# Performance work log

Measured on AMD Instinct MI355X. Metric: run time of the kernel, lower is better.

## Reference

```python
import jax, jax.numpy as jnp
import numpy as np

CH = 128
GROUPS = 8
EPS = 1e-5


def setup_inputs() -> dict:
    key = jax.random.key(0)
    ks = jax.random.split(key, 12)
    b, c, h, w = 16, CH, 64, 64
    x = jax.random.normal(ks[0], (b, c, h, w), dtype=jnp.float32)
    s = 1.0 / np.sqrt(c)
    return {
        "x": x,
        "gn_w": jnp.ones((c,), jnp.float32),
        "gn_b": jnp.zeros((c,), jnp.float32),
        "wq": jax.random.normal(ks[1], (c, c), jnp.float32) * s,
        "bq": jax.random.normal(ks[2], (c,), jnp.float32) * 0.01,
        "wk": jax.random.normal(ks[3], (c, c), jnp.float32) * s,
        "bk": jax.random.normal(ks[4], (c,), jnp.float32) * 0.01,
        "wv": jax.random.normal(ks[5], (c, c), jnp.float32) * s,
        "bv": jax.random.normal(ks[6], (c,), jnp.float32) * 0.01,
        "wf": jax.random.normal(ks[7], (c, c), jnp.float32) * s,
        "bf": jax.random.normal(ks[8], (c,), jnp.float32) * 0.01,
    }


def _group_norm(x, gamma, beta):
    b, c, h, w = x.shape
    xg = x.reshape(b, GROUPS, -1)  # [b, g, (c/g)*h*w]
    mean = xg.mean(axis=-1, keepdims=True)
    var = xg.var(axis=-1, keepdims=True)
    xn = ((xg - mean) * jax.lax.rsqrt(var + EPS)).reshape(b, c, h, w)
    return xn * gamma[None, :, None, None] + beta[None, :, None, None]


def reference(x, gn_w, gn_b, wq, bq, wk, bk, wv, bv, wf, bf):
    b, c, h, w = x.shape
    x_gn = _group_norm(x, gn_w, gn_b)
    xf = x_gn.reshape(b, c, h * w)  # [b, c, n]
    # 1x1 convs == per-position channel matmuls
    q = jnp.einsum('oc,bcn->bon', wq, xf) + bq[None, :, None]
    k = jnp.einsum('oc,bcn->bon', wk, xf) + bk[None, :, None]
    v = jnp.einsum('oc,bcn->bon', wv, xf) + bv[None, :, None]
    scale = c ** (-0.5)
    attn = jnp.einsum('bci,bcj->bij', q, k) * scale  # [b, n, n]
    attn = jax.nn.softmax(attn, axis=-1)
    # out[b,c,i] = sum_j v[b,c,j] * attn[b,i,j]
    o = jnp.einsum('bcj,bij->bci', v, attn)
    of = jnp.einsum('oc,bcn->bon', wf, o) + bf[None, :, None]
    return of.reshape(b, c, h, w) + x
```

## Files before the change

### kernel.cpp

```cpp
#include <hip/hip_runtime.h>

#define NB   16
#define NC   128
#define NPOS 4096

typedef short bf16x8 __attribute__((ext_vector_type(8)));
typedef float f32x4  __attribute__((ext_vector_type(4)));
typedef float f32x16 __attribute__((ext_vector_type(16)));
typedef unsigned int u32x4 __attribute__((ext_vector_type(4)));

#define SCF 0.12751743075095855f

static __device__ __forceinline__ unsigned short f2bf(float f) {
    unsigned int u = __builtin_bit_cast(unsigned int, f);
    u += 0x7FFFu + ((u >> 16) & 1u);
    return (unsigned short)(u >> 16);
}

static __device__ __forceinline__ unsigned int pkbf(float hi, float lo) {
    return __builtin_amdgcn_perm(__builtin_bit_cast(unsigned int, hi),
                                 __builtin_bit_cast(unsigned int, lo), 0x07060302u);
}

static __device__ __forceinline__ float vmax16(const f32x16 v) {
    float a = fmaxf(fmaxf(v[0], v[1]), fmaxf(v[2], v[3]));
    float b = fmaxf(fmaxf(v[4], v[5]), fmaxf(v[6], v[7]));
    float c = fmaxf(fmaxf(v[8], v[9]), fmaxf(v[10], v[11]));
    float d = fmaxf(fmaxf(v[12], v[13]), fmaxf(v[14], v[15]));
    return fmaxf(fmaxf(a, b), fmaxf(c, d));
}

static __device__ __forceinline__ float vsum16(const float* p) {
    float a = (p[0] + p[1]) + (p[2] + p[3]);
    float b = (p[4] + p[5]) + (p[6] + p[7]);
    float c = (p[8] + p[9]) + (p[10] + p[11]);
    float d = (p[12] + p[13]) + (p[14] + p[15]);
    return (a + b) + (c + d);
}

static __device__ __forceinline__ void mk_bfrag_pair(const float* pp, bf16x8* dst, int h) {
    #pragma unroll
    for (int c2 = 0; c2 < 2; ++c2) {
        int rb = c2 * 8;
        unsigned int A0 = pkbf(pp[rb + 1], pp[rb + 0]);
        unsigned int A1 = pkbf(pp[rb + 3], pp[rb + 2]);
        unsigned int B0 = pkbf(pp[rb + 5], pp[rb + 4]);
        unsigned int B1 = pkbf(pp[rb + 7], pp[rb + 6]);
        unsigned int s0 = h ? A0 : B0, s1 = h ? A1 : B1;
        unsigned int r0 = __shfl_xor(s0, 32), r1 = __shfl_xor(s1, 32);
        u32x4 f;
        f[0] = h ? r0 : A0; f[1] = h ? r1 : A1;
        f[2] = h ? B0 : r0; f[3] = h ? B1 : r1;
        dst[c2] = __builtin_bit_cast(bf16x8, f);
    }
}

__global__ void wconv_kernel(const float* __restrict__ wq, const float* __restrict__ wk,
                             const float* __restrict__ wv, const float* __restrict__ wf,
                             unsigned short* __restrict__ oq, unsigned short* __restrict__ ok,
                             unsigned short* __restrict__ ov, unsigned short* __restrict__ of) {
    int i = blockIdx.x * 256 + threadIdx.x;
    oq[i] = f2bf(wq[i]); ok[i] = f2bf(wk[i]); ov[i] = f2bf(wv[i]); of[i] = f2bf(wf[i]);
}

__global__ void gnstat_kernel(const float* __restrict__ x, float* __restrict__ mean,
                              float* __restrict__ rstd) {
    int bg = blockIdx.x;
    const float* p = x + (size_t)bg * 65536;
    int t = threadIdx.x;
    float s = 0.f, q = 0.f;
    for (int it = 0; it < 64; ++it) {
        f32x4 v = *(const f32x4*)(p + it * 1024 + t * 4);
        s += v[0] + v[1] + v[2] + v[3];
        q += v[0] * v[0] + v[1] * v[1] + v[2] * v[2] + v[3] * v[3];
    }
    for (int m = 1; m < 64; m <<= 1) { s += __shfl_xor(s, m); q += __shfl_xor(q, m); }
    __shared__ float ls[4], lq[4];
    int w = t >> 6;
    if ((t & 63) == 0) { ls[w] = s; lq[w] = q; }
    __syncthreads();
    if (t == 0) {
        s = ls[0] + ls[1] + ls[2] + ls[3];
        q = lq[0] + lq[1] + lq[2] + lq[3];
        float mu  = s * (1.0f / 65536.0f);
        float var = q * (1.0f / 65536.0f) - mu * mu;
        mean[bg] = mu;
        rstd[bg] = rsqrtf(var + 1e-5f);
    }
}

__global__ __launch_bounds__(256) void qkv_kernel(
    const float* __restrict__ x, const float* __restrict__ gnw, const float* __restrict__ gnb,
    const float* __restrict__ mean, const float* __restrict__ rstd,
    const unsigned short* __restrict__ wqb, const unsigned short* __restrict__ wkb,
    const unsigned short* __restrict__ wvb,
    const float* __restrict__ bq, const float* __restrict__ bk, const float* __restrict__ bv,
    unsigned short* __restrict__ qT, unsigned short* __restrict__ Kf, unsigned short* __restrict__ Vf) {
    __shared__ __attribute__((aligned(16))) unsigned short xn[64 * 136];
    __shared__ __attribute__((aligned(16))) unsigned short bnc[64 * 128];
    const int b = blockIdx.y, i0 = blockIdx.x * 64, jt = blockIdx.x;
    const int t = threadIdx.x;
    {
        int iL = (t & 15) * 4;
        int cb = (t >> 4) * 2;
        for (int cg = 0; cg < 4; ++cg) {
            int c = cg * 32 + cb;
            int g = c >> 4;
            float mu = mean[b * 8 + g], rs = rstd[b * 8 + g];
            float ga0 = gnw[c] * rs,     be0 = gnb[c]     - mu * ga0;
            float ga1 = gnw[c + 1] * rs, be1 = gnb[c + 1] - mu * ga1;
            const float* p0 = x + ((size_t)(b * NC + c)) * NPOS + i0 + iL;
            f32x4 v0 = *(const f32x4*)p0;
            f32x4 v1 = *(const f32x4*)(p0 + NPOS);
            for (int e = 0; e < 4; ++e) {
                unsigned int u = (unsigned)f2bf(v0[e] * ga0 + be0) |
                                 ((unsigned)f2bf(v1[e] * ga1 + be1) << 16);
                *(unsigned int*)&xn[(iL + e) * 136 + c] = u;
            }
        }
    }
    __syncthreads();

    const int lane = t & 63, w = t >> 6, quad = lane >> 4, li = lane & 15;

    bf16x8 ax[4];
    for (int kc = 0; kc < 4; ++kc)
        ax[kc] = *(const bf16x8*)&xn[(w * 16 + li) * 136 + kc * 32 + quad * 8];

    for (int wt = 0; wt < 2; ++wt) {
        const unsigned short* W = wt ? wkb : wqb;
        const float* bias = wt ? bk : bq;
        const float osc = wt ? 1.0f : SCF;
        for (int nt = 0; nt < 8; ++nt) {
            f32x4 d = {0.f, 0.f, 0.f, 0.f};
            for (int kc = 0; kc < 4; ++kc) {
                bf16x8 bw = *(const bf16x8*)&W[(nt * 16 + li) * 128 + kc * 32 + quad * 8];
                d = __builtin_amdgcn_mfma_f32_16x16x32_bf16(ax[kc], bw, d, 0, 0, 0);
            }
            float bb = bias[nt * 16 + li];
            int o = nt * 16 + li;
            for (int rr = 0; rr < 4; ++rr) {
                int i = w * 16 + quad * 4 + rr;
                bnc[i * 128 + (((o >> 3) ^ (i & 7)) << 3) + (o & 7)] = f2bf((d[rr] + bb) * osc);
            }
        }
        __syncthreads();
        if (wt == 0) {
            unsigned short* dst = qT + ((size_t)b * NPOS + i0) * NC + t * 32;
            int i = t >> 2;
            for (int s = 0; s < 4; ++s) {
                int cc = (t & 3) * 4 + s;
                *(bf16x8*)(dst + s * 8) = *(const bf16x8*)&bnc[i * 128 + ((cc ^ (i & 7)) << 3)];
            }
        } else {
            unsigned short* dst = Kf + ((size_t)(b * 64 + jt)) * 8192 + t * 32;
            int F = t >> 4, jtile = F >> 3, kc = F & 7;
            for (int s = 0; s < 4; ++s) {
                int L = (t * 4 + s) & 63;
                int i = jtile * 32 + (L & 31);
                int cc = kc * 2 + (L >> 5);
                *(bf16x8*)(dst + s * 8) = *(const bf16x8*)&bnc[i * 128 + ((cc ^ (i & 7)) << 3)];
            }
        }
        __syncthreads();
    }

    bf16x8 av[2][4];
    for (int mt = 0; mt < 2; ++mt)
        for (int kc = 0; kc < 4; ++kc)
            av[mt][kc] = *(const bf16x8*)&wvb[((w * 2 + mt) * 16 + li) * 128 + kc * 32 + quad * 8];
    for (int nt = 0; nt < 4; ++nt) {
        bf16x8 bx[4];
        for (int kc = 0; kc < 4; ++kc)
            bx[kc] = *(const bf16x8*)&xn[(nt * 16 + li) * 136 + kc * 32 + quad * 8];
        for (int mt = 0; mt < 2; ++mt) {
            f32x4 d = {0.f, 0.f, 0.f, 0.f};
            for (int kc = 0; kc < 4; ++kc)
                d = __builtin_amdgcn_mfma_f32_16x16x32_bf16(av[mt][kc], bx[kc], d, 0, 0, 0);
            int o0 = (w * 2 + mt) * 16 + quad * 4;
            int j = nt * 16 + li;
            for (int rr = 0; rr < 4; ++rr) {
                int c = o0 + rr;
                bnc[c * 64 + (((j >> 3) ^ (c & 7)) << 3) + (j & 7)] = f2bf(d[rr] + bv[c]);
            }
        }
    }
    __syncthreads();
    {
        unsigned short* dst = Vf + ((size_t)(b * 64 + jt)) * 8192 + t * 32;
        int F = t >> 4, ct = F >> 2, kc2 = F & 3;
        for (int s = 0; s < 4; ++s) {
            int L = (t * 4 + s) & 63;
            int c = ct * 32 + (L & 31);
            int jc = kc2 * 2 + (L >> 5);
            *(bf16x8*)(dst + s * 8) = *(const bf16x8*)&bnc[c * 64 + ((jc ^ (c & 7)) << 3)];
        }
    }
}

__global__ __launch_bounds__(256, 2) void flash_kernel(
    const unsigned short* __restrict__ qT, const unsigned short* __restrict__ Kf,
    const unsigned short* __restrict__ Vf, const unsigned short* __restrict__ wfb,
    const float* __restrict__ bf_, const float* __restrict__ x, float* __restrict__ out) {
    const int idx = blockIdx.x;
    const int b = (idx & 7) * 2 + ((idx >> 3) & 1);
    const int rg = idx >> 4;
    const int t = threadIdx.x, lane = t & 63, w = t >> 6;
    const int il = lane & 31, h = lane >> 5;
    const int iw = (rg * 4 + w) * 32;

    bf16x8 qb[8];
    #pragma unroll
    for (int kc = 0; kc < 8; ++kc)
        qb[kc] = *(const bf16x8*)&qT[((size_t)b * NPOS + iw + il) * NC + kc * 16 + h * 8];

    float mr = -1e30f, lr = 0.f;
    f32x16 acc[4];
    #pragma unroll
    for (int ct = 0; ct < 4; ++ct)
        #pragma unroll
        for (int q = 0; q < 16; ++q) acc[ct][q] = 0.f;

    const unsigned short* kp = Kf + ((size_t)b * 64) * 8192 + lane * 8;
    const unsigned short* vp = Vf + ((size_t)b * 64) * 8192 + lane * 8;

    bf16x8 kf[16];
    #pragma unroll
    for (int m = 0; m < 16; ++m) kf[m] = *(const bf16x8*)(kp + m * 512);
    kp += 8192;

    for (int jt = 0; jt < 64; ++jt) {
        f32x16 st[2];
        #pragma unroll
        for (int u = 0; u < 2; ++u)
            #pragma unroll
            for (int q = 0; q < 16; ++q) st[u][q] = 0.f;
        #pragma unroll
        for (int kc = 0; kc < 8; ++kc) {
            st[0] = __builtin_amdgcn_mfma_f32_32x32x16_bf16(kf[kc],     qb[kc], st[0], 0, 0, 0);
            st[1] = __builtin_amdgcn_mfma_f32_32x32x16_bf16(kf[8 + kc], qb[kc], st[1], 0, 0, 0);
        }
        #pragma unroll
        for (int m = 0; m < 16; ++m) kf[m] = *(const bf16x8*)(kp + m * 512);
        kp += 8192;

        float mx = fmaxf(vmax16(st[0]), vmax16(st[1]));
        mx = fmaxf(mx, __shfl_xor(mx, 32));
        if (__any(mx > mr)) {
            float mn = fmaxf(mr, mx);
            float alpha = __builtin_amdgcn_exp2f(mr - mn);
            mr = mn;
            lr *= alpha;
            #pragma unroll
            for (int ct = 0; ct < 4; ++ct)
                #pragma unroll
                for (int q = 0; q < 16; ++q) acc[ct][q] *= alpha;
        }
        float mc = mr - 0.0028150156f;
        #pragma unroll
        for (int q = 0; q < 16; ++q) {
            st[0][q] = __builtin_amdgcn_exp2f(st[0][q] - mc);
            st[1][q] = __builtin_amdgcn_exp2f(st[1][q] - mc);
        }
        float rs = vsum16((const float*)&st[0]) + vsum16((const float*)&st[1]);
        rs += __shfl_xor(rs, 32);
        lr += rs;

        bf16x8 pfrag[4];
        mk_bfrag_pair((const float*)&st[0], &pfrag[0], h);
        mk_bfrag_pair((const float*)&st[1], &pfrag[2], h);

        bf16x8 vf[16];
        #pragma unroll
        for (int m = 0; m < 16; ++m) vf[m] = *(const bf16x8*)(vp + m * 512);
        vp += 8192;

        #pragma unroll
        for (int ct = 0; ct < 4; ++ct)
            #pragma unroll
            for (int kc2 = 0; kc2 < 4; ++kc2)
                acc[ct] = __builtin_amdgcn_mfma_f32_32x32x16_bf16(vf[ct * 4 + kc2], pfrag[kc2],
                                                                  acc[ct], 0, 0, 0);
    }

    bf16x8 obf[8];
    {
        float inv = __builtin_amdgcn_rcpf(lr) * 1.001953125f;
        #pragma unroll
        for (int ct = 0; ct < 4; ++ct) {
            float pp[16];
            #pragma unroll
            for (int q = 0; q < 16; ++q) pp[q] = acc[ct][q] * inv;
            mk_bfrag_pair(pp, &obf[ct * 2], h);
        }
    }

    #pragma unroll
    for (int ot = 0; ot < 4; ++ot) {
        bf16x8 wfA[8];
        #pragma unroll
        for (int kc = 0; kc < 8; ++kc)
            wfA[kc] = *(const bf16x8*)&wfb[(ot * 32 + il) * 128 + kc * 16 + h * 8];
        f32x16 d;
        #pragma unroll
        for (int q = 0; q < 16; ++q) d[q] = 0.f;
        #pragma unroll
        for (int kc = 0; kc < 8; ++kc)
            d = __builtin_amdgcn_mfma_f32_32x32x16_bf16(wfA[kc], obf[kc], d, 0, 0, 0);
        const int gi = iw + il;
        #pragma unroll
        for (int q = 0; q < 16; ++q) {
            int o = ot * 32 + (q & 3) + 8 * (q >> 2) + 4 * h;
            size_t a = ((size_t)(b * NC + o)) * NPOS + gi;
            out[a] = d[q] + bf_[o] + x[a];
        }
    }
}

extern "C" void kernel_launch(void* const* d_in, const int* in_sizes, int n_in,
                              void* d_out, int out_size, void* d_ws, size_t ws_size,
                              hipStream_t stream) {
    const float* x   = (const float*)d_in[0];
    const float* gnw = (const float*)d_in[1];
    const float* gnb = (const float*)d_in[2];
    const float* wq  = (const float*)d_in[3];
    const float* bq  = (const float*)d_in[4];
    const float* wk  = (const float*)d_in[5];
    const float* bk  = (const float*)d_in[6];
    const float* wv  = (const float*)d_in[7];
    const float* bv  = (const float*)d_in[8];
    const float* wf  = (const float*)d_in[9];
    const float* bf_ = (const float*)d_in[10];
    float* out = (float*)d_out;

    char* ws = (char*)d_ws;
    float* mean = (float*)(ws + 0);
    float* rstd = (float*)(ws + 512);
    unsigned short* wqb = (unsigned short*)(ws + 1024);
    unsigned short* wkb = wqb + 16384;
    unsigned short* wvb = wkb + 16384;
    unsigned short* wfb = wvb + 16384;
    unsigned short* qT  = (unsigned short*)(ws + 132096);
    unsigned short* Kf  = qT + (size_t)NB * NPOS * NC;
    unsigned short* Vf  = Kf + (size_t)NB * NPOS * NC;

    wconv_kernel<<<64, 256, 0, stream>>>(wq, wk, wv, wf, wqb, wkb, wvb, wfb);
    gnstat_kernel<<<128, 256, 0, stream>>>(x, mean, rstd);
    dim3 g(64, 16);
    qkv_kernel<<<g, 256, 0, stream>>>(x, gnw, gnb, mean, rstd, wqb, wkb, wvb, bq, bk, bv, qT, Kf, Vf);
    flash_kernel<<<512, 256, 0, stream>>>(qT, Kf, Vf, wfb, bf_, x, out);
}
```

Measured before the change: 341.5 us.

## Stage K/V tiles in double-buffered LDS via direct global-to-LDS loads

Each of the four waves used to load every K and V tile from global memory into its own registers. Now the block shares the tiles through a double-buffered LDS area filled with global_load_lds, and the next tile is prefetched while the current one is used. The MFMA sections are also wrapped in s_setprio. This cuts redundant global and L2 traffic and register pressure. In exchange it adds 64KB of LDS per block (which may limit occupancy at two blocks per CU), a __syncthreads per iteration, and LDS read latency inside the MFMA chains.

Measured after the change: 315.3 us. 7.7% less time.

```diff
diff --git a/kernel.cpp b/kernel.cpp
--- a/kernel.cpp
+++ b/kernel.cpp
@@ -52,6 +52,17 @@
         f[0] = h ? r0 : A0; f[1] = h ? r1 : A1;
         f[2] = h ? B0 : r0; f[3] = h ? B1 : r1;
         dst[c2] = __builtin_bit_cast(bf16x8, f);
+    }
+}
+
+static __device__ __forceinline__ void stage_tile(unsigned short* lds, const unsigned short* g,
+                                                  int t, int w) {
+    #pragma unroll
+    for (int c = 0; c < 4; ++c) {
+        __builtin_amdgcn_global_load_lds(
+            (const __attribute__((address_space(1))) unsigned int*)(g + c * 2048 + t * 8),
+            (__attribute__((address_space(3))) unsigned int*)(lds + c * 2048 + w * 512),
+            16, 0, 0);
     }
 }
 
@@ -202,6 +213,7 @@
     const unsigned short* __restrict__ qT, const unsigned short* __restrict__ Kf,
     const unsigned short* __restrict__ Vf, const unsigned short* __restrict__ wfb,
     const float* __restrict__ bf_, const float* __restrict__ x, float* __restrict__ out) {
+    __shared__ __attribute__((aligned(16))) unsigned short KV[2][2][8192];
     const int idx = blockIdx.x;
     const int b = (idx & 7) * 2 + ((idx >> 3) & 1);
     const int rg = idx >> 4;
@@ -209,6 +221,12 @@
     const int il = lane & 31, h = lane >> 5;
     const int iw = (rg * 4 + w) * 32;
 
+    const unsigned short* Kb = Kf + ((size_t)b * 64) * 8192;
+    const unsigned short* Vb = Vf + ((size_t)b * 64) * 8192;
+
+    stage_tile(&KV[0][0][0], Kb, t, w);
+    stage_tile(&KV[0][1][0], Vb, t, w);
+
     bf16x8 qb[8];
     #pragma unroll
     for (int kc = 0; kc < 8; ++kc)
@@ -221,28 +239,31 @@
         #pragma unroll
         for (int q = 0; q < 16; ++q) acc[ct][q] = 0.f;
 
-    const unsigned short* kp = Kf + ((size_t)b * 64) * 8192 + lane * 8;
-    const unsigned short* vp = Vf + ((size_t)b * 64) * 8192 + lane * 8;
-
-    bf16x8 kf[16];
-    #pragma unroll
-    for (int m = 0; m < 16; ++m) kf[m] = *(const bf16x8*)(kp + m * 512);
-    kp += 8192;
+    __syncthreads();
 
     for (int jt = 0; jt < 64; ++jt) {
+        const int cur = jt & 1;
+        const unsigned short* kl = &KV[cur][0][0] + lane * 8;
+        const unsigned short* vl = &KV[cur][1][0] + lane * 8;
+        if (jt < 63) {
+            stage_tile(&KV[cur ^ 1][0][0], Kb + (size_t)(jt + 1) * 8192, t, w);
+            stage_tile(&KV[cur ^ 1][1][0], Vb + (size_t)(jt + 1) * 8192, t, w);
+        }
+
         f32x16 st[2];
         #pragma unroll
         for (int u = 0; u < 2; ++u)
             #pragma unroll
             for (int q = 0; q < 16; ++q) st[u][q] = 0.f;
+        __builtin_amdgcn_s_setprio(1);
         #pragma unroll
         for (int kc = 0; kc < 8; ++kc) {
-            st[0] = __builtin_amdgcn_mfma_f32_32x32x16_bf16(kf[kc],     qb[kc], st[0], 0, 0, 0);
-            st[1] = __builtin_amdgcn_mfma_f32_32x32x16_bf16(kf[8 + kc], qb[kc], st[1], 0, 0, 0);
-        }
-        #pragma unroll
-        for (int m = 0; m < 16; ++m) kf[m] = *(const bf16x8*)(kp + m * 512);
-        kp += 8192;
+            bf16x8 k0 = *(const bf16x8*)(kl + kc * 512);
+            bf16x8 k1 = *(const bf16x8*)(kl + (8 + kc) * 512);
+            st[0] = __builtin_amdgcn_mfma_f32_32x32x16_bf16(k0, qb[kc], st[0], 0, 0, 0);
+            st[1] = __builtin_amdgcn_mfma_f32_32x32x16_bf16(k1, qb[kc], st[1], 0, 0, 0);
+        }
+        __builtin_amdgcn_s_setprio(0);
 
         float mx = fmaxf(vmax16(st[0]), vmax16(st[1]));
         mx = fmaxf(mx, __shfl_xor(mx, 32));
@@ -270,17 +291,18 @@
         mk_bfrag_pair((const float*)&st[0], &pfrag[0], h);
         mk_bfrag_pair((const float*)&st[1], &pfrag[2], h);
 
-        bf16x8 vf[16];
-        #pragma unroll
-        for (int m = 0; m < 16; ++m) vf[m] = *(const bf16x8*)(vp + m * 512);
-        vp += 8192;
-
+        __builtin_amdgcn_s_setprio(1);
         #pragma unroll
         for (int ct = 0; ct < 4; ++ct)
             #pragma unroll
-            for (int kc2 = 0; kc2 < 4; ++kc2)
-                acc[ct] = __builtin_amdgcn_mfma_f32_32x32x16_bf16(vf[ct * 4 + kc2], pfrag[kc2],
+            for (int kc2 = 0; kc2 < 4; ++kc2) {
+                bf16x8 vfm = *(const bf16x8*)(vl + (ct * 4 + kc2) * 512);
+                acc[ct] = __builtin_amdgcn_mfma_f32_32x32x16_bf16(vfm, pfrag[kc2],
                                                                   acc[ct], 0, 0, 0);
+            }
+        __builtin_amdgcn_s_setprio(0);
+
+        __syncthreads();
     }
 
     bf16x8 obf[8];
```
